# Optimization experiments

Hardware: AMD Instinct MI355X
Metric: run time of the kernel (lower is better)

Reference implementation:

```python
import jax, jax.numpy as jnp
import numpy as np

B = 262144
IN_FEATURES = 128
OUT_FEATURES = 128
NQ_IN = IN_FEATURES // 4
NQ_OUT = OUT_FEATURES // 4


def setup_inputs() -> dict:
    key = jax.random.key(0)
    kx, kw, kb = jax.random.split(key, 3)
    stdv = 1.0 / np.sqrt(IN_FEATURES).astype(np.float32)
    x = jax.random.normal(kx, (B, IN_FEATURES), dtype=jnp.float32)
    weight = jax.random.uniform(kw, (NQ_OUT, NQ_IN, 4), dtype=jnp.float32,
                                minval=-stdv, maxval=stdv)
    bias = jax.random.uniform(kb, (OUT_FEATURES,), dtype=jnp.float32,
                              minval=-stdv, maxval=stdv)
    return {"x": x, "weight": weight, "bias": bias}


def reference(x, weight, bias):
    b = x.shape[0]
    nq_in = weight.shape[1]
    # [B, nq_in, 4] quaternion components
    xq = x.reshape(b, nq_in, 4)
    xa, xi, xj, xk = xq[..., 0], xq[..., 1], xq[..., 2], xq[..., 3]
    wa, wi, wj, wk = weight[..., 0], weight[..., 1], weight[..., 2], weight[..., 3]
    # each term: [B, nq_in] @ [nq_in, nq_out] -> [B, nq_out]
    mm = lambda u, w: jnp.einsum('bn,on->bo', u, w)
    out_a = mm(xa, wa) - mm(xi, wi) - mm(xj, wj) - mm(xk, wk)
    out_i = mm(xa, wi) + mm(xi, wa) + mm(xj, wk) - mm(xk, wj)
    out_j = mm(xa, wj) - mm(xi, wk) + mm(xj, wa) + mm(xk, wi)
    out_k = mm(xa, wk) + mm(xi, wj) - mm(xj, wi) + mm(xk, wa)
    out = jnp.stack([out_a, out_i, out_j, out_k], axis=-1).reshape(b, -1)
    return out + bias
```

## Files before the change

### kernel.cpp

```cpp
#include <hip/hip_runtime.h>
#include <hip/hip_bf16.h>

typedef __bf16 bf16x8 __attribute__((ext_vector_type(8)));
typedef float  f32x4  __attribute__((ext_vector_type(4)));

#define NTILES      16384
#define GEMM_BLOCKS 2048

__global__ __launch_bounds__(256) void prep_wfrag(const float* __restrict__ w,
                                                  ushort* __restrict__ wfrag) {
    int t = blockIdx.x * 256 + threadIdx.x;
    if (t >= 128 * 128) return;
    int j    = t & 7;
    int lane = (t >> 3) & 63;
    int kb   = (t >> 9) & 3;
    int nt   = t >> 11;
    int g    = lane >> 4;
    int n = nt * 16 + (lane & 15);
    int k = kb * 32 + (j < 4 ? g * 4 + j : 16 + g * 4 + (j - 4));
    int o  = n >> 2, c = n & 3;
    int nq = k >> 2, d = k & 3;
    int comp = c ^ d;
    bool neg = (d != 0) && ((c == 0) || (c != d && d != (c % 3) + 1));
    float val = w[o * 128 + nq * 4 + comp];
    val = neg ? -val : val;
    __bf16 bv = (__bf16)val;
    wfrag[t] = *reinterpret_cast<ushort*>(&bv);
}

__global__ __launch_bounds__(512, 8) void qgemm(const float* __restrict__ x,
                                                const ushort* __restrict__ wfrag,
                                                const float* __restrict__ bias,
                                                float* __restrict__ out) {
    __shared__ __align__(16) ushort wlds[16384];
    __shared__ __align__(16) float  sbias[128];

    int tid   = threadIdx.x;
    int lane  = tid & 63;
    int wid   = tid >> 6;
    int row16 = lane & 15;
    int kgrp  = lane >> 4;

    int4 wtmp[4];
    {
        const int4* src = (const int4*)wfrag;
#pragma unroll
        for (int i = 0; i < 4; ++i) wtmp[i] = src[tid + i * 512];
    }

    size_t tile = (size_t)blockIdx.x * 8 + wid;
    const float4* xv = (const float4*)(x + tile * 2048 + row16 * 128);
    float4 r[8];
#pragma unroll
    for (int kb = 0; kb < 4; ++kb) {
        r[2 * kb]     = xv[kb * 8 + kgrp];
        r[2 * kb + 1] = xv[kb * 8 + kgrp + 4];
    }

    {
        int4* dst = (int4*)wlds;
#pragma unroll
        for (int i = 0; i < 4; ++i) dst[tid + i * 512] = wtmp[i];
    }
    if (tid < 128) sbias[tid] = bias[tid];
    __syncthreads();

    bf16x8 afr[4];
#pragma unroll
    for (int kb = 0; kb < 4; ++kb) {
        float4 p = r[2 * kb], q = r[2 * kb + 1];
        afr[kb][0] = (__bf16)p.x; afr[kb][1] = (__bf16)p.y;
        afr[kb][2] = (__bf16)p.z; afr[kb][3] = (__bf16)p.w;
        afr[kb][4] = (__bf16)q.x; afr[kb][5] = (__bf16)q.y;
        afr[kb][6] = (__bf16)q.z; afr[kb][7] = (__bf16)q.w;
    }

    const bf16x8* blds = (const bf16x8*)wlds;
    float* op = out + tile * 2048 + row16 * 128 + kgrp * 4;
#pragma unroll
    for (int nt = 0; nt < 8; ++nt) {
        f32x4 acc = *(const f32x4*)&sbias[nt * 16 + kgrp * 4];
#pragma unroll
        for (int kb = 0; kb < 4; ++kb) {
            bf16x8 wfr = blds[(nt * 4 + kb) * 64 + lane];
            acc = __builtin_amdgcn_mfma_f32_16x16x32_bf16(wfr, afr[kb], acc, 0, 0, 0);
        }
        *(f32x4*)(op + nt * 16) = acc;
    }
}

extern "C" void kernel_launch(void* const* d_in, const int* in_sizes, int n_in,
                              void* d_out, int out_size, void* d_ws, size_t ws_size,
                              hipStream_t stream) {
    const float* x      = (const float*)d_in[0];
    const float* weight = (const float*)d_in[1];
    const float* bias   = (const float*)d_in[2];
    float*       out    = (float*)d_out;
    ushort*      wfrag  = (ushort*)d_ws;

    prep_wfrag<<<64, 256, 0, stream>>>(weight, wfrag);
    qgemm<<<GEMM_BLOCKS, 512, 0, stream>>>(x, wfrag, bias, out);
}
```

Before: 55.89 us.

## Make GEMM waves persistent over four tiles with double-buffered x loads

```diff
diff --git a/kernel.cpp b/kernel.cpp
--- a/kernel.cpp
+++ b/kernel.cpp
@@ -4,8 +4,8 @@
 typedef __bf16 bf16x8 __attribute__((ext_vector_type(8)));
 typedef float  f32x4  __attribute__((ext_vector_type(4)));
 
-#define NTILES      16384
-#define GEMM_BLOCKS 2048
+#define NTILES 16384
+#define NWAVES 4096
 
 __global__ __launch_bounds__(256) void prep_wfrag(const float* __restrict__ w,
                                                   ushort* __restrict__ wfrag) {
@@ -28,65 +28,75 @@
     wfrag[t] = *reinterpret_cast<ushort*>(&bv);
 }
 
-__global__ __launch_bounds__(512, 8) void qgemm(const float* __restrict__ x,
+__global__ __launch_bounds__(256, 4) void qgemm(const float* __restrict__ x,
                                                 const ushort* __restrict__ wfrag,
                                                 const float* __restrict__ bias,
                                                 float* __restrict__ out) {
     __shared__ __align__(16) ushort wlds[16384];
     __shared__ __align__(16) float  sbias[128];
 
-    int tid   = threadIdx.x;
+    int tid = threadIdx.x;
+    {
+        const int4* src = (const int4*)wfrag;
+        int4*       dst = (int4*)wlds;
+#pragma unroll
+        for (int i = 0; i < 8; ++i) dst[tid + i * 256] = src[tid + i * 256];
+    }
+    if (tid < 128) sbias[tid] = bias[tid];
+
     int lane  = tid & 63;
     int wid   = tid >> 6;
     int row16 = lane & 15;
     int kgrp  = lane >> 4;
+    int loff  = row16 * 128 + kgrp * 4;
 
-    int4 wtmp[4];
-    {
-        const int4* src = (const int4*)wfrag;
-#pragma unroll
-        for (int i = 0; i < 4; ++i) wtmp[i] = src[tid + i * 512];
-    }
-
-    size_t tile = (size_t)blockIdx.x * 8 + wid;
-    const float4* xv = (const float4*)(x + tile * 2048 + row16 * 128);
-    float4 r[8];
-#pragma unroll
-    for (int kb = 0; kb < 4; ++kb) {
-        r[2 * kb]     = xv[kb * 8 + kgrp];
-        r[2 * kb + 1] = xv[kb * 8 + kgrp + 4];
-    }
-
-    {
-        int4* dst = (int4*)wlds;
-#pragma unroll
-        for (int i = 0; i < 4; ++i) dst[tid + i * 512] = wtmp[i];
-    }
-    if (tid < 128) sbias[tid] = bias[tid];
     __syncthreads();
 
-    bf16x8 afr[4];
-#pragma unroll
-    for (int kb = 0; kb < 4; ++kb) {
-        float4 p = r[2 * kb], q = r[2 * kb + 1];
-        afr[kb][0] = (__bf16)p.x; afr[kb][1] = (__bf16)p.y;
-        afr[kb][2] = (__bf16)p.z; afr[kb][3] = (__bf16)p.w;
-        afr[kb][4] = (__bf16)q.x; afr[kb][5] = (__bf16)q.y;
-        afr[kb][6] = (__bf16)q.z; afr[kb][7] = (__bf16)q.w;
-    }
+    const bf16x8* blds = (const bf16x8*)wlds;
+    int g = blockIdx.x * 4 + wid;
 
-    const bf16x8* blds = (const bf16x8*)wlds;
-    float* op = out + tile * 2048 + row16 * 128 + kgrp * 4;
-#pragma unroll
-    for (int nt = 0; nt < 8; ++nt) {
-        f32x4 acc = *(const f32x4*)&sbias[nt * 16 + kgrp * 4];
+    float4 rA[8], rB[8];
+
+    auto load_tile = [&](float4* r, int t) {
+        const float4* xv = (const float4*)(x + (size_t)t * 2048 + loff);
 #pragma unroll
         for (int kb = 0; kb < 4; ++kb) {
-            bf16x8 wfr = blds[(nt * 4 + kb) * 64 + lane];
-            acc = __builtin_amdgcn_mfma_f32_16x16x32_bf16(wfr, afr[kb], acc, 0, 0, 0);
+            r[2 * kb]     = xv[kb * 8];
+            r[2 * kb + 1] = xv[kb * 8 + 4];
         }
-        *(f32x4*)(op + nt * 16) = acc;
-    }
+    };
+
+    auto compute_tile = [&](const float4* r, int t) {
+        bf16x8 afr[4];
+#pragma unroll
+        for (int kb = 0; kb < 4; ++kb) {
+            float4 p = r[2 * kb], q = r[2 * kb + 1];
+            afr[kb][0] = (__bf16)p.x; afr[kb][1] = (__bf16)p.y;
+            afr[kb][2] = (__bf16)p.z; afr[kb][3] = (__bf16)p.w;
+            afr[kb][4] = (__bf16)q.x; afr[kb][5] = (__bf16)q.y;
+            afr[kb][6] = (__bf16)q.z; afr[kb][7] = (__bf16)q.w;
+        }
+        float* op = out + (size_t)t * 2048 + loff;
+#pragma unroll
+        for (int nt = 0; nt < 8; ++nt) {
+            f32x4 acc = *(const f32x4*)&sbias[nt * 16 + kgrp * 4];
+#pragma unroll
+            for (int kb = 0; kb < 4; ++kb) {
+                bf16x8 wfr = blds[(nt * 4 + kb) * 64 + lane];
+                acc = __builtin_amdgcn_mfma_f32_16x16x32_bf16(wfr, afr[kb], acc, 0, 0, 0);
+            }
+            *(f32x4*)(op + nt * 16) = acc;
+        }
+    };
+
+    load_tile(rA, g);
+    load_tile(rB, g + NWAVES);
+    compute_tile(rA, g);
+    load_tile(rA, g + 2 * NWAVES);
+    compute_tile(rB, g + NWAVES);
+    load_tile(rB, g + 3 * NWAVES);
+    compute_tile(rA, g + 2 * NWAVES);
+    compute_tile(rB, g + 3 * NWAVES);
 }
 
 extern "C" void kernel_launch(void* const* d_in, const int* in_sizes, int n_in,
@@ -99,5 +109,5 @@
     ushort*      wfrag  = (ushort*)d_ws;
 
     prep_wfrag<<<64, 256, 0, stream>>>(weight, wfrag);
-    qgemm<<<GEMM_BLOCKS, 512, 0, stream>>>(x, wfrag, bias, out);
+    qgemm<<<1024, 256, 0, stream>>>(x, wfrag, bias, out);
 }
```

Result: slower. 66.73 us (+19.4%).

## Stage output tile through swizzled LDS for coalesced nontemporal stores, halve block size

Applied to the files above, without the earlier changes.

```diff
diff --git a/kernel.cpp b/kernel.cpp
--- a/kernel.cpp
+++ b/kernel.cpp
@@ -4,8 +4,7 @@
 typedef __bf16 bf16x8 __attribute__((ext_vector_type(8)));
 typedef float  f32x4  __attribute__((ext_vector_type(4)));
 
-#define NTILES      16384
-#define GEMM_BLOCKS 2048
+#define NTILES 16384
 
 __global__ __launch_bounds__(256) void prep_wfrag(const float* __restrict__ w,
                                                   ushort* __restrict__ wfrag) {
@@ -28,7 +27,7 @@
     wfrag[t] = *reinterpret_cast<ushort*>(&bv);
 }
 
-__global__ __launch_bounds__(512, 8) void qgemm(const float* __restrict__ x,
+__global__ __launch_bounds__(256, 4) void qgemm(const float* __restrict__ x,
                                                 const ushort* __restrict__ wfrag,
                                                 const float* __restrict__ bias,
                                                 float* __restrict__ out) {
@@ -40,27 +39,28 @@
     int wid   = tid >> 6;
     int row16 = lane & 15;
     int kgrp  = lane >> 4;
+    int loff  = row16 * 128 + kgrp * 4;
 
-    int4 wtmp[4];
+    int4 wtmp[8];
     {
         const int4* src = (const int4*)wfrag;
 #pragma unroll
-        for (int i = 0; i < 4; ++i) wtmp[i] = src[tid + i * 512];
+        for (int i = 0; i < 8; ++i) wtmp[i] = src[tid + i * 256];
     }
 
-    size_t tile = (size_t)blockIdx.x * 8 + wid;
-    const float4* xv = (const float4*)(x + tile * 2048 + row16 * 128);
+    size_t tile = (size_t)blockIdx.x * 4 + wid;
+    const float4* xv = (const float4*)(x + tile * 2048 + loff);
     float4 r[8];
 #pragma unroll
     for (int kb = 0; kb < 4; ++kb) {
-        r[2 * kb]     = xv[kb * 8 + kgrp];
-        r[2 * kb + 1] = xv[kb * 8 + kgrp + 4];
+        r[2 * kb]     = xv[kb * 8];
+        r[2 * kb + 1] = xv[kb * 8 + 4];
     }
 
     {
         int4* dst = (int4*)wlds;
 #pragma unroll
-        for (int i = 0; i < 4; ++i) dst[tid + i * 512] = wtmp[i];
+        for (int i = 0; i < 8; ++i) dst[tid + i * 256] = wtmp[i];
     }
     if (tid < 128) sbias[tid] = bias[tid];
     __syncthreads();
@@ -76,16 +76,36 @@
     }
 
     const bf16x8* blds = (const bf16x8*)wlds;
-    float* op = out + tile * 2048 + row16 * 128 + kgrp * 4;
+    f32x4 acc[8];
 #pragma unroll
     for (int nt = 0; nt < 8; ++nt) {
-        f32x4 acc = *(const f32x4*)&sbias[nt * 16 + kgrp * 4];
+        acc[nt] = *(const f32x4*)&sbias[nt * 16 + kgrp * 4];
 #pragma unroll
         for (int kb = 0; kb < 4; ++kb) {
             bf16x8 wfr = blds[(nt * 4 + kb) * 64 + lane];
-            acc = __builtin_amdgcn_mfma_f32_16x16x32_bf16(wfr, afr[kb], acc, 0, 0, 0);
+            acc[nt] = __builtin_amdgcn_mfma_f32_16x16x32_bf16(wfr, afr[kb], acc[nt], 0, 0, 0);
         }
-        *(f32x4*)(op + nt * 16) = acc;
+    }
+
+    __syncthreads();
+
+    float* stg = (float*)wlds + wid * 2048;
+#pragma unroll
+    for (int nt = 0; nt < 8; ++nt) {
+        int c = nt * 4 + kgrp;
+        *(f32x4*)(stg + row16 * 128 + ((c ^ (row16 & 7)) << 2)) = acc[nt];
+    }
+    asm volatile("s_waitcnt lgkmcnt(0)" ::: "memory");
+    __builtin_amdgcn_sched_barrier(0);
+
+    f32x4* ob = (f32x4*)(out + tile * 2048);
+#pragma unroll
+    for (int s = 0; s < 8; ++s) {
+        int p   = lane + 64 * s;
+        int row = p >> 5;
+        int c   = p & 31;
+        f32x4 v = *(const f32x4*)(stg + row * 128 + ((c ^ (row & 7)) << 2));
+        __builtin_nontemporal_store(v, ob + p);
     }
 }
 
@@ -99,5 +119,5 @@
     ushort*      wfrag  = (ushort*)d_ws;
 
     prep_wfrag<<<64, 256, 0, stream>>>(weight, wfrag);
-    qgemm<<<GEMM_BLOCKS, 512, 0, stream>>>(x, wfrag, bias, out);
+    qgemm<<<4096, 256, 0, stream>>>(x, wfrag, bias, out);
 }
```

New measurement: 49.22 us, median of 2. -11.9%, faster.
